# Kernel tuning notes

Measured on AMD Instinct MI355X. Metric: run time of the kernel, lower is better.

## Reference

```python
import jax, jax.numpy as jnp
import numpy as np

EMBED_DIM = 1024
NUM_HEADS = 16
HEAD_DIM = EMBED_DIM // NUM_HEADS
B, T, S = 4, 2048, 2048


def setup_inputs() -> dict:
    key = jax.random.key(0)
    ks = jax.random.split(key, 11)
    sd = 1.0 / np.sqrt(EMBED_DIM)
    inp = {
        "query": jax.random.normal(ks[0], (B, T, EMBED_DIM), jnp.float32),
        "key": jax.random.normal(ks[1], (B, S, EMBED_DIM), jnp.float32),
        "value": jax.random.normal(ks[2], (B, S, EMBED_DIM), jnp.float32),
        # torch nn.Linear weights have shape (out_features, in_features)
        "Wq": jax.random.normal(ks[3], (EMBED_DIM, EMBED_DIM), jnp.float32) * sd,
        "bq": jnp.zeros((EMBED_DIM,), jnp.float32),
        "Wk": jax.random.normal(ks[4], (EMBED_DIM, EMBED_DIM), jnp.float32) * sd,
        "bk": jnp.zeros((EMBED_DIM,), jnp.float32),
        "Wv": jax.random.normal(ks[5], (EMBED_DIM, EMBED_DIM), jnp.float32) * sd,
        "bv": jnp.zeros((EMBED_DIM,), jnp.float32),
        "Wo": jax.random.normal(ks[6], (EMBED_DIM, EMBED_DIM), jnp.float32) * sd,
        "bo": jnp.zeros((EMBED_DIM,), jnp.float32),
    }
    return inp


def reference(query, key, value, Wq, bq, Wk, bk, Wv, bv, Wo, bo):
    scale = HEAD_DIM ** -0.5
    # projections (torch Linear: x @ W.T + b)
    q = query @ Wq.T + bq  # (B,T,C)
    k = key @ Wk.T + bk    # (B,S,C)
    v = value @ Wv.T + bv  # (B,S,C)
    # split heads -> (B,H,T,D)
    q = q.reshape(B, T, NUM_HEADS, HEAD_DIM).transpose(0, 2, 1, 3)
    k = k.reshape(B, S, NUM_HEADS, HEAD_DIM).transpose(0, 2, 1, 3)
    v = v.reshape(B, S, NUM_HEADS, HEAD_DIM).transpose(0, 2, 1, 3)
    # scores (B,H,T,S), softmax, weighted sum (dropout p=0 -> identity)
    scores = jnp.einsum("bhtd,bhsd->bhts", q, k) * scale
    attn = jax.nn.softmax(scores, axis=-1)
    out = jnp.einsum("bhts,bhsd->bhtd", attn, v)
    out = out.transpose(0, 2, 1, 3).reshape(B, T, EMBED_DIM)
    return out @ Wo.T + bo
```

## Files before the change

### kernel.cpp

```cpp
#include <hip/hip_runtime.h>
#include <math.h>
#include <stdint.h>

#define EMBED 1024
#define HEADS 16
#define HDIM  64
#define BATCH 4
#define SEQL  2048
#define MROWS (BATCH*SEQL)

typedef unsigned short u16;
typedef __bf16 bf16x8 __attribute__((ext_vector_type(8)));
typedef float  f32x16 __attribute__((ext_vector_type(16)));
typedef u16    u16x8  __attribute__((ext_vector_type(8)));

using gu32 = const __attribute__((address_space(1))) uint32_t;
using lu32 = __attribute__((address_space(3))) uint32_t;

__device__ __forceinline__ u16 f2b(float f) {
  union { float f; uint32_t u; } c; c.f = f;
  return (u16)((c.u + 0x7fffu + ((c.u >> 16) & 1u)) >> 16);
}
__device__ __forceinline__ uint32_t pk2(float lo, float hi) {
  return (uint32_t)f2b(lo) | ((uint32_t)f2b(hi) << 16);
}

__global__ void cvt_bf16(const float* __restrict__ in, u16* __restrict__ out, int n4) {
  int i = blockIdx.x * blockDim.x + threadIdx.x;
  const int stride = gridDim.x * blockDim.x;
  for (; i < n4; i += stride) {
    float4 v = reinterpret_cast<const float4*>(in)[i];
    ushort4 o;
    o.x = f2b(v.x); o.y = f2b(v.y); o.z = f2b(v.z); o.w = f2b(v.w);
    reinterpret_cast<ushort4*>(out)[i] = o;
  }
}

template<int MODE>
__global__ __launch_bounds__(256)
void gemm_bf16(const u16* __restrict__ A, const u16* __restrict__ W,
               const float* __restrict__ bias, void* __restrict__ outp, float scale)
{
  __shared__ __attribute__((aligned(16))) u16 As[128 * 64];
  __shared__ __attribute__((aligned(16))) u16 Bs[128 * 64];
  const int tid  = threadIdx.x;
  const int lane = tid & 63;
  const int wid  = tid >> 6;
  const int wm = wid >> 1, wn = wid & 1;
  const int l31 = lane & 31, hh = lane >> 5;
  const int bm = blockIdx.x * 128, bn = blockIdx.y * 128;

  f32x16 acc[2][2] = {};

  for (int k0 = 0; k0 < EMBED; k0 += 64) {
    __syncthreads();
#pragma unroll
    for (int r = 0; r < 4; ++r) {
      const int u = tid + r * 256;
      const int row = u >> 3, c = u & 7;
      __builtin_amdgcn_global_load_lds(
          (gu32*)(A + (size_t)(bm + row) * EMBED + k0 + c * 8),
          (lu32*)(As + (size_t)u * 8), 16, 0, 0);
      __builtin_amdgcn_global_load_lds(
          (gu32*)(W + (size_t)(bn + row) * EMBED + k0 + c * 8),
          (lu32*)(Bs + (size_t)u * 8), 16, 0, 0);
    }
    __syncthreads();

#pragma unroll
    for (int g = 0; g < 4; ++g) {
      bf16x8 af[2], bfr[2];
#pragma unroll
      for (int it = 0; it < 2; ++it) {
        const int row = wm * 64 + it * 32 + l31;
        af[it] = *reinterpret_cast<const bf16x8*>(As + row * 64 + g * 16 + hh * 8);
      }
#pragma unroll
      for (int jt = 0; jt < 2; ++jt) {
        const int row = wn * 64 + jt * 32 + l31;
        bfr[jt] = *reinterpret_cast<const bf16x8*>(Bs + row * 64 + g * 16 + hh * 8);
      }
#pragma unroll
      for (int it = 0; it < 2; ++it)
#pragma unroll
        for (int jt = 0; jt < 2; ++jt)
          acc[it][jt] = __builtin_amdgcn_mfma_f32_32x32x16_bf16(af[it], bfr[jt], acc[it][jt], 0, 0, 0);
    }
  }

#pragma unroll
  for (int it = 0; it < 2; ++it)
#pragma unroll
    for (int jt = 0; jt < 2; ++jt) {
      const int n = bn + wn * 64 + jt * 32 + l31;
      const float bv = bias[n];
#pragma unroll
      for (int reg = 0; reg < 16; ++reg) {
        const int m = bm + wm * 64 + it * 32 + (reg & 3) + 8 * (reg >> 2) + 4 * hh;
        const float val = (acc[it][jt][reg] + bv) * scale;
        if (MODE == 0) {
          ((float*)outp)[(size_t)m * EMBED + n] = val;
        } else {
          const int b = m >> 11, t = m & (SEQL - 1);
          const int h = n >> 6,  d = n & (HDIM - 1);
          ((u16*)outp)[(((size_t)(b * HEADS + h)) * SEQL + t) * HDIM + d] = f2b(val);
        }
      }
    }
}

__global__ __launch_bounds__(256)
void attn_mfma(const u16* __restrict__ Qp, const u16* __restrict__ Kp,
               const u16* __restrict__ Vp, u16* __restrict__ Ob)
{
  __shared__ __attribute__((aligned(16))) u16 smem[128 * 66];
  u16* Ks = smem;
  u16* Vt = smem + 4096;

  const int tid  = threadIdx.x;
  const int lane = tid & 63;
  const int wq   = tid >> 6;
  const int l31  = lane & 31, hh = lane >> 5;
  const int bh   = blockIdx.y;
  const int q0   = blockIdx.x * 128;
  const size_t kvbase = (size_t)bh * SEQL * HDIM;

  bf16x8 qf[4];
  {
    const u16* qrow = Qp + kvbase + (size_t)(q0 + wq * 32 + l31) * HDIM;
#pragma unroll
    for (int g = 0; g < 4; ++g)
      qf[g] = *reinterpret_cast<const bf16x8*>(qrow + g * 16 + hh * 8);
  }

  float mrow = -INFINITY, lrow = 0.f;
  f32x16 oacc[2] = {};

  for (int s0 = 0; s0 < SEQL; s0 += 64) {
    __syncthreads();
#pragma unroll
    for (int r = 0; r < 2; ++r) {
      const int u = tid + r * 256;
      const int s = u >> 3, cc = u & 7;
      const int cg = cc ^ (s & 7);
      __builtin_amdgcn_global_load_lds(
          (gu32*)(Kp + kvbase + (size_t)(s0 + s) * HDIM + cg * 8),
          (lu32*)(Ks + (size_t)u * 8), 16, 0, 0);
    }
    u16x8 vreg[2];
#pragma unroll
    for (int r = 0; r < 2; ++r) {
      const int u = tid + r * 256;
      const int s = u >> 3, c = u & 7;
      vreg[r] = *reinterpret_cast<const u16x8*>(Vp + kvbase + (size_t)(s0 + s) * HDIM + c * 8);
    }
#pragma unroll
    for (int r = 0; r < 2; ++r) {
      const int u = tid + r * 256;
      const int s = u >> 3, c = u & 7;
#pragma unroll
      for (int e = 0; e < 8; ++e) {
        const int d = c * 8 + e;
        const int slot = (s >> 3) ^ (d & 7) ^ (d >> 3);
        Vt[d * 64 + slot * 8 + (s & 7)] = vreg[r][e];
      }
    }
    __syncthreads();

    f32x16 st[2] = {};
#pragma unroll
    for (int ts = 0; ts < 2; ++ts) {
      const int srow = ts * 32 + l31;
#pragma unroll
      for (int g = 0; g < 4; ++g) {
        const int slot = (g * 2 + hh) ^ (srow & 7);
        bf16x8 kf = *reinterpret_cast<const bf16x8*>(Ks + srow * 64 + slot * 8);
        st[ts] = __builtin_amdgcn_mfma_f32_32x32x16_bf16(kf, qf[g], st[ts], 0, 0, 0);
      }
    }

    float mx = -INFINITY;
#pragma unroll
    for (int ts = 0; ts < 2; ++ts)
#pragma unroll
      for (int rg = 0; rg < 16; ++rg) mx = fmaxf(mx, st[ts][rg]);
    mx = fmaxf(mx, __shfl_xor(mx, 32));
    const float mnew = fmaxf(mrow, mx);
    const float alpha = __expf(mrow - mnew);
    float rsum = 0.f;
#pragma unroll
    for (int ts = 0; ts < 2; ++ts)
#pragma unroll
      for (int rg = 0; rg < 16; ++rg) {
        const float p = __expf(st[ts][rg] - mnew);
        st[ts][rg] = p;
        rsum += p;
      }
    rsum += __shfl_xor(rsum, 32);
    lrow = lrow * alpha + rsum;
    mrow = mnew;
#pragma unroll
    for (int jd = 0; jd < 2; ++jd)
#pragma unroll
      for (int rg = 0; rg < 16; ++rg) oacc[jd][rg] *= alpha;

    bf16x8 pb[4];
#pragma unroll
    for (int ts = 0; ts < 2; ++ts)
#pragma unroll
      for (int gl = 0; gl < 2; ++gl) {
        const int rb = gl * 8;
        const uint32_t A0 = pk2(st[ts][rb + 0], st[ts][rb + 1]);
        const uint32_t A1 = pk2(st[ts][rb + 2], st[ts][rb + 3]);
        const uint32_t B0 = pk2(st[ts][rb + 4], st[ts][rb + 5]);
        const uint32_t B1 = pk2(st[ts][rb + 6], st[ts][rb + 7]);
        const uint32_t sA0 = __shfl_xor(A0, 32);
        const uint32_t sA1 = __shfl_xor(A1, 32);
        const uint32_t sB0 = __shfl_xor(B0, 32);
        const uint32_t sB1 = __shfl_xor(B1, 32);
        union { uint32_t w[4]; bf16x8 v; } f;
        f.w[0] = hh ? sB0 : A0;
        f.w[1] = hh ? sB1 : A1;
        f.w[2] = hh ? B0  : sA0;
        f.w[3] = hh ? B1  : sA1;
        pb[ts * 2 + gl] = f.v;
      }

#pragma unroll
    for (int gs = 0; gs < 4; ++gs)
#pragma unroll
      for (int jd = 0; jd < 2; ++jd) {
        const int drow = jd * 32 + l31;
        const int slot = (gs * 2 + hh) ^ (drow & 7) ^ (drow >> 3);
        bf16x8 vf = *reinterpret_cast<const bf16x8*>(Vt + drow * 64 + slot * 8);
        oacc[jd] = __builtin_amdgcn_mfma_f32_32x32x16_bf16(vf, pb[gs], oacc[jd], 0, 0, 0);
      }
  }

  __syncthreads();
  u16* Os = smem;
  const float inv = 1.f / lrow;
  const int trow = wq * 32 + l31;
#pragma unroll
  for (int jd = 0; jd < 2; ++jd)
#pragma unroll
    for (int q = 0; q < 4; ++q) {
      const int dbase = jd * 32 + 8 * q + 4 * hh;
      const uint32_t w0 = pk2(oacc[jd][q * 4 + 0] * inv, oacc[jd][q * 4 + 1] * inv);
      const uint32_t w1 = pk2(oacc[jd][q * 4 + 2] * inv, oacc[jd][q * 4 + 3] * inv);
      *reinterpret_cast<uint32_t*>(Os + trow * 66 + dbase)     = w0;
      *reinterpret_cast<uint32_t*>(Os + trow * 66 + dbase + 2) = w1;
    }
  __syncthreads();
  const int b = bh >> 4, h = bh & 15;
#pragma unroll
  for (int r = 0; r < 4; ++r) {
    const int u = tid + r * 256;
    const int row = u >> 3, c = u & 7;
    uint32_t wds[4];
#pragma unroll
    for (int i2 = 0; i2 < 4; ++i2)
      wds[i2] = *reinterpret_cast<const uint32_t*>(Os + row * 66 + c * 8 + i2 * 2);
    uint4 ov; ov.x = wds[0]; ov.y = wds[1]; ov.z = wds[2]; ov.w = wds[3];
    *reinterpret_cast<uint4*>(Ob + ((size_t)(b * SEQL + q0 + row)) * EMBED + h * 64 + c * 8) = ov;
  }
}

extern "C" void kernel_launch(void* const* d_in, const int* in_sizes, int n_in,
                              void* d_out, int out_size, void* d_ws, size_t ws_size,
                              hipStream_t stream)
{
  const float* query = (const float*)d_in[0];
  const float* key   = (const float*)d_in[1];
  const float* value = (const float*)d_in[2];
  const float* Wq    = (const float*)d_in[3];
  const float* bq    = (const float*)d_in[4];
  const float* Wk    = (const float*)d_in[5];
  const float* bk    = (const float*)d_in[6];
  const float* Wv    = (const float*)d_in[7];
  const float* bv    = (const float*)d_in[8];
  const float* Wo    = (const float*)d_in[9];
  const float* bo    = (const float*)d_in[10];
  float* out = (float*)d_out;

  const size_t NBIG = (size_t)1 << 23;
  const size_t NW   = (size_t)1 << 20;
  u16* Xq  = (u16*)d_ws;
  u16* Xk  = Xq  + NBIG;
  u16* Xv  = Xk  + NBIG;
  u16* Wqb = Xv  + NBIG;
  u16* Wkb = Wqb + NW;
  u16* Wvb = Wkb + NW;
  u16* Wob = Wvb + NW;
  u16* Qb  = Wob + NW;
  u16* Kb  = Qb  + NBIG;
  u16* Vb  = Kb  + NBIG;
  u16* Oa  = Vb  + NBIG;

  cvt_bf16<<<2048, 256, 0, stream>>>(query, Xq, (int)(NBIG / 4));
  cvt_bf16<<<2048, 256, 0, stream>>>(key,   Xk, (int)(NBIG / 4));
  cvt_bf16<<<2048, 256, 0, stream>>>(value, Xv, (int)(NBIG / 4));
  cvt_bf16<<<512,  256, 0, stream>>>(Wq, Wqb, (int)(NW / 4));
  cvt_bf16<<<512,  256, 0, stream>>>(Wk, Wkb, (int)(NW / 4));
  cvt_bf16<<<512,  256, 0, stream>>>(Wv, Wvb, (int)(NW / 4));
  cvt_bf16<<<512,  256, 0, stream>>>(Wo, Wob, (int)(NW / 4));

  const dim3 gg(MROWS / 128, EMBED / 128);
  gemm_bf16<1><<<gg, 256, 0, stream>>>(Xq, Wqb, bq, Qb, 0.125f);
  gemm_bf16<1><<<gg, 256, 0, stream>>>(Xk, Wkb, bk, Kb, 1.f);
  gemm_bf16<1><<<gg, 256, 0, stream>>>(Xv, Wvb, bv, Vb, 1.f);

  attn_mfma<<<dim3(SEQL / 128, BATCH * HEADS), 256, 0, stream>>>(Qb, Kb, Vb, Oa);

  gemm_bf16<0><<<gg, 256, 0, stream>>>(Oa, Wob, bo, out, 1.f);
}
```

Measured before the change: 461.0 us.

## Batch QKV GEMMs, widen GEMM blocks, use exp2 with lazy softmax rescale

Merges the three projection GEMMs into one launch over a z grid dimension and raises the GEMM blocks to 512 threads, with each wave now owning a 64x32 tile. The attention softmax switches to exp2, with log2(e) folded into the Q scale. It also skips the running-max rescale while the new max stays within 8 of the old one. The bf16 conversion now uses the native __bf16 cast. The goal is less launch overhead, cheaper exponentials and less accumulator rescaling. The trade-offs are less register reuse per wave in the GEMM and a possible rounding difference in the conversion.

```diff
diff --git a/kernel.cpp b/kernel.cpp
--- a/kernel.cpp
+++ b/kernel.cpp
@@ -17,12 +17,15 @@
 using gu32 = const __attribute__((address_space(1))) uint32_t;
 using lu32 = __attribute__((address_space(3))) uint32_t;
 
+#define LOG2E 1.44269504088896340736f
+
 __device__ __forceinline__ u16 f2b(float f) {
-  union { float f; uint32_t u; } c; c.f = f;
-  return (u16)((c.u + 0x7fffu + ((c.u >> 16) & 1u)) >> 16);
+  union { __bf16 h; u16 u; } c; c.h = (__bf16)f; return c.u;
 }
 __device__ __forceinline__ uint32_t pk2(float lo, float hi) {
-  return (uint32_t)f2b(lo) | ((uint32_t)f2b(hi) << 16);
+  union { __bf16 h[2]; uint32_t u; } c;
+  c.h[0] = (__bf16)lo; c.h[1] = (__bf16)hi;
+  return c.u;
 }
 
 __global__ void cvt_bf16(const float* __restrict__ in, u16* __restrict__ out, int n4) {
@@ -30,33 +33,32 @@
   const int stride = gridDim.x * blockDim.x;
   for (; i < n4; i += stride) {
     float4 v = reinterpret_cast<const float4*>(in)[i];
-    ushort4 o;
-    o.x = f2b(v.x); o.y = f2b(v.y); o.z = f2b(v.z); o.w = f2b(v.w);
-    reinterpret_cast<ushort4*>(out)[i] = o;
+    uint2 o; o.x = pk2(v.x, v.y); o.y = pk2(v.z, v.w);
+    reinterpret_cast<uint2*>(out)[i] = o;
   }
 }
 
 template<int MODE>
-__global__ __launch_bounds__(256)
-void gemm_bf16(const u16* __restrict__ A, const u16* __restrict__ W,
-               const float* __restrict__ bias, void* __restrict__ outp, float scale)
-{
-  __shared__ __attribute__((aligned(16))) u16 As[128 * 64];
-  __shared__ __attribute__((aligned(16))) u16 Bs[128 * 64];
+__device__ __forceinline__ void gemm_core(const u16* __restrict__ A,
+                                          const u16* __restrict__ W,
+                                          const float* __restrict__ bias,
+                                          void* __restrict__ outp, float scale,
+                                          u16* As, u16* Bs)
+{
   const int tid  = threadIdx.x;
   const int lane = tid & 63;
   const int wid  = tid >> 6;
-  const int wm = wid >> 1, wn = wid & 1;
+  const int wm = wid >> 2, wn = wid & 3;
   const int l31 = lane & 31, hh = lane >> 5;
   const int bm = blockIdx.x * 128, bn = blockIdx.y * 128;
 
-  f32x16 acc[2][2] = {};
+  f32x16 acc[2] = {};
 
   for (int k0 = 0; k0 < EMBED; k0 += 64) {
     __syncthreads();
 #pragma unroll
-    for (int r = 0; r < 4; ++r) {
-      const int u = tid + r * 256;
+    for (int r = 0; r < 2; ++r) {
+      const int u = tid + r * 512;
       const int row = u >> 3, c = u & 7;
       __builtin_amdgcn_global_load_lds(
           (gu32*)(A + (size_t)(bm + row) * EMBED + k0 + c * 8),
@@ -69,44 +71,66 @@
 
 #pragma unroll
     for (int g = 0; g < 4; ++g) {
-      bf16x8 af[2], bfr[2];
+      bf16x8 af[2], bfr;
 #pragma unroll
       for (int it = 0; it < 2; ++it) {
         const int row = wm * 64 + it * 32 + l31;
         af[it] = *reinterpret_cast<const bf16x8*>(As + row * 64 + g * 16 + hh * 8);
       }
-#pragma unroll
-      for (int jt = 0; jt < 2; ++jt) {
-        const int row = wn * 64 + jt * 32 + l31;
-        bfr[jt] = *reinterpret_cast<const bf16x8*>(Bs + row * 64 + g * 16 + hh * 8);
+      {
+        const int row = wn * 32 + l31;
+        bfr = *reinterpret_cast<const bf16x8*>(Bs + row * 64 + g * 16 + hh * 8);
       }
 #pragma unroll
       for (int it = 0; it < 2; ++it)
-#pragma unroll
-        for (int jt = 0; jt < 2; ++jt)
-          acc[it][jt] = __builtin_amdgcn_mfma_f32_32x32x16_bf16(af[it], bfr[jt], acc[it][jt], 0, 0, 0);
-    }
-  }
-
-#pragma unroll
-  for (int it = 0; it < 2; ++it)
-#pragma unroll
-    for (int jt = 0; jt < 2; ++jt) {
-      const int n = bn + wn * 64 + jt * 32 + l31;
-      const float bv = bias[n];
-#pragma unroll
-      for (int reg = 0; reg < 16; ++reg) {
-        const int m = bm + wm * 64 + it * 32 + (reg & 3) + 8 * (reg >> 2) + 4 * hh;
-        const float val = (acc[it][jt][reg] + bv) * scale;
-        if (MODE == 0) {
-          ((float*)outp)[(size_t)m * EMBED + n] = val;
-        } else {
-          const int b = m >> 11, t = m & (SEQL - 1);
-          const int h = n >> 6,  d = n & (HDIM - 1);
-          ((u16*)outp)[(((size_t)(b * HEADS + h)) * SEQL + t) * HDIM + d] = f2b(val);
-        }
-      }
-    }
+        acc[it] = __builtin_amdgcn_mfma_f32_32x32x16_bf16(af[it], bfr, acc[it], 0, 0, 0);
+    }
+  }
+
+  const int n = bn + wn * 32 + l31;
+  const float bv = bias[n];
+#pragma unroll
+  for (int it = 0; it < 2; ++it) {
+#pragma unroll
+    for (int reg = 0; reg < 16; ++reg) {
+      const int m = bm + wm * 64 + it * 32 + (reg & 3) + 8 * (reg >> 2) + 4 * hh;
+      const float val = (acc[it][reg] + bv) * scale;
+      if (MODE == 0) {
+        ((float*)outp)[(size_t)m * EMBED + n] = val;
+      } else {
+        const int b = m >> 11, t = m & (SEQL - 1);
+        const int h = n >> 6,  d = n & (HDIM - 1);
+        ((u16*)outp)[(((size_t)(b * HEADS + h)) * SEQL + t) * HDIM + d] = f2b(val);
+      }
+    }
+  }
+}
+
+__global__ __launch_bounds__(512)
+void gemm_qkv(const u16* __restrict__ A0, const u16* __restrict__ A1, const u16* __restrict__ A2,
+              const u16* __restrict__ W0, const u16* __restrict__ W1, const u16* __restrict__ W2,
+              const float* __restrict__ b0, const float* __restrict__ b1, const float* __restrict__ b2,
+              u16* __restrict__ o0, u16* __restrict__ o1, u16* __restrict__ o2,
+              float s0)
+{
+  __shared__ __attribute__((aligned(16))) u16 As[128 * 64];
+  __shared__ __attribute__((aligned(16))) u16 Bs[128 * 64];
+  const int z = blockIdx.z;
+  const u16*   A = (z == 0) ? A0 : (z == 1) ? A1 : A2;
+  const u16*   W = (z == 0) ? W0 : (z == 1) ? W1 : W2;
+  const float* b = (z == 0) ? b0 : (z == 1) ? b1 : b2;
+  u16*         o = (z == 0) ? o0 : (z == 1) ? o1 : o2;
+  const float  s = (z == 0) ? s0 : 1.f;
+  gemm_core<1>(A, W, b, o, s, As, Bs);
+}
+
+__global__ __launch_bounds__(512)
+void gemm_out(const u16* __restrict__ A, const u16* __restrict__ W,
+              const float* __restrict__ bias, float* __restrict__ outp)
+{
+  __shared__ __attribute__((aligned(16))) u16 As[128 * 64];
+  __shared__ __attribute__((aligned(16))) u16 Bs[128 * 64];
+  gemm_core<0>(A, W, bias, outp, 1.f, As, Bs);
 }
 
 __global__ __launch_bounds__(256)
@@ -185,24 +209,27 @@
 #pragma unroll
       for (int rg = 0; rg < 16; ++rg) mx = fmaxf(mx, st[ts][rg]);
     mx = fmaxf(mx, __shfl_xor(mx, 32));
-    const float mnew = fmaxf(mrow, mx);
-    const float alpha = __expf(mrow - mnew);
+    if (!__all(mx <= mrow + 8.f)) {
+      const float mnew = fmaxf(mrow, mx);
+      const float alpha = __builtin_amdgcn_exp2f(mrow - mnew);
+      lrow *= alpha;
+#pragma unroll
+      for (int jd = 0; jd < 2; ++jd)
+#pragma unroll
+        for (int rg = 0; rg < 16; ++rg) oacc[jd][rg] *= alpha;
+      mrow = mnew;
+    }
     float rsum = 0.f;
 #pragma unroll
     for (int ts = 0; ts < 2; ++ts)
 #pragma unroll
       for (int rg = 0; rg < 16; ++rg) {
-        const float p = __expf(st[ts][rg] - mnew);
+        const float p = __builtin_amdgcn_exp2f(st[ts][rg] - mrow);
         st[ts][rg] = p;
         rsum += p;
       }
     rsum += __shfl_xor(rsum, 32);
-    lrow = lrow * alpha + rsum;
-    mrow = mnew;
-#pragma unroll
-    for (int jd = 0; jd < 2; ++jd)
-#pragma unroll
-      for (int rg = 0; rg < 16; ++rg) oacc[jd][rg] *= alpha;
+    lrow += rsum;
 
     bf16x8 pb[4];
 #pragma unroll
@@ -305,12 +332,11 @@
   cvt_bf16<<<512,  256, 0, stream>>>(Wv, Wvb, (int)(NW / 4));
   cvt_bf16<<<512,  256, 0, stream>>>(Wo, Wob, (int)(NW / 4));
 
-  const dim3 gg(MROWS / 128, EMBED / 128);
-  gemm_bf16<1><<<gg, 256, 0, stream>>>(Xq, Wqb, bq, Qb, 0.125f);
-  gemm_bf16<1><<<gg, 256, 0, stream>>>(Xk, Wkb, bk, Kb, 1.f);
-  gemm_bf16<1><<<gg, 256, 0, stream>>>(Xv, Wvb, bv, Vb, 1.f);
+  gemm_qkv<<<dim3(MROWS / 128, EMBED / 128, 3), 512, 0, stream>>>(
+      Xq, Xk, Xv, Wqb, Wkb, Wvb, bq, bk, bv, Qb, Kb, Vb,
+      0.125f * LOG2E);
 
   attn_mfma<<<dim3(SEQL / 128, BATCH * HEADS), 256, 0, stream>>>(Qb, Kb, Vb, Oa);
 
-  gemm_bf16<0><<<gg, 256, 0, stream>>>(Oa, Wob, bo, out, 1.f);
-}
+  gemm_out<<<dim3(MROWS / 128, EMBED / 128), 512, 0, stream>>>(Oa, Wob, bo, out);
+}
```

Measured after the change: 496.1 us. 1.08x slower.
